# Optimization experiments

Measured on AMD Instinct MI355X. Metric: run time of the kernel, lower is better.

## Reference

```python
import jax, jax.numpy as jnp
import numpy as np

D_MODEL = 1024
N_HEADS = 16
HEAD_DIM = D_MODEL // N_HEADS


def setup_inputs() -> dict:
    key = jax.random.key(0)
    ks = jax.random.split(key, 5)
    T, B = 2048, 2
    scale = 1.0 / np.sqrt(D_MODEL)
    x = jax.random.normal(ks[0], (T, B, D_MODEL), dtype=jnp.float32)
    W_qkv = jax.random.normal(ks[1], (D_MODEL, 3 * D_MODEL), dtype=jnp.float32) * scale
    b_qkv = jnp.zeros((3 * D_MODEL,), dtype=jnp.float32)
    W_out = jax.random.normal(ks[2], (D_MODEL, D_MODEL), dtype=jnp.float32) * scale
    b_out = jnp.zeros((D_MODEL,), dtype=jnp.float32)
    return {"x": x, "W_qkv": W_qkv, "b_qkv": b_qkv, "W_out": W_out, "b_out": b_out}


def reference(x, W_qkv, b_qkv, W_out, b_out):
    T, B, D = x.shape
    H, Dh = N_HEADS, HEAD_DIM
    qkv = x @ W_qkv + b_qkv  # [T, B, 3D]
    q, k, v = jnp.split(qkv, 3, axis=-1)
    # [T, B, D] -> [B, H, T, Dh]
    def to_heads(t):
        return t.reshape(T, B, H, Dh).transpose(1, 2, 0, 3)
    q, k, v = to_heads(q), to_heads(k), to_heads(v)
    scores = jnp.einsum("bhqd,bhkd->bhqk", q, k) / jnp.sqrt(jnp.float32(Dh))
    causal = jnp.tril(jnp.ones((T, T), dtype=bool))  # True where attention allowed
    scores = jnp.where(causal, scores, -jnp.inf)
    attn = jax.nn.softmax(scores, axis=-1)
    context = jnp.einsum("bhqk,bhkd->bhqd", attn, v)  # [B, H, T, Dh]
    context = context.transpose(2, 0, 1, 3).reshape(T, B, D)  # [T, B, D]
    return context @ W_out + b_out
```

## Files before the change

kernel.cpp:

```cpp
#include <hip/hip_runtime.h>
#include <stdint.h>

#define T_SEQ 2048
#define BATCH 2
#define DMODEL 1024
#define NH 16
#define DH 64
#define M_ROWS (T_SEQ * BATCH)
#define N_QKV (3 * DMODEL)
#define BHQ (32 * T_SEQ)

typedef unsigned short u16;
using bf16x8 = __attribute__((ext_vector_type(8))) __bf16;
using f32x4  = __attribute__((ext_vector_type(4))) float;

__device__ __forceinline__ u16 f2bf(float f) {
    union { float f; uint32_t u; } v; v.f = f;
    uint32_t r = v.u + 0x7fffu + ((v.u >> 16) & 1u);
    return (u16)(r >> 16);
}

__device__ __forceinline__ uint32_t pack2(float a, float b) {
    union { float f; uint32_t u; } x, y; x.f = a; y.f = b;
    return (x.u >> 16) | (y.u & 0xffff0000u);
}

__device__ __forceinline__ float bf2f(u16 u) {
    union { uint32_t u; float f; } v; v.u = (uint32_t)u << 16;
    return v.f;
}

__device__ __forceinline__ void lds_load16(void* lds, const void* g) {
    auto lp = (__attribute__((address_space(3))) uint32_t*)(uint32_t)(uintptr_t)lds;
    auto gp = (const __attribute__((address_space(1))) uint32_t*)(uintptr_t)g;
    __builtin_amdgcn_global_load_lds(gp, lp, 16, 0, 0);
}

#define SCQ 0.18033688011112f


__global__ void cvt4_kernel(const float* __restrict__ in, u16* __restrict__ out, int n4) {
    int i = blockIdx.x * 256 + threadIdx.x;
    if (i < n4) {
        float4 v = ((const float4*)in)[i];
        union { u16 u[4]; uint2 d; } o;
        o.u[0] = f2bf(v.x); o.u[1] = f2bf(v.y); o.u[2] = f2bf(v.z); o.u[3] = f2bf(v.w);
        ((uint2*)out)[i] = o.d;
    }
}

__global__ void cvt_t2_kernel(const float* __restrict__ A, u16* __restrict__ oA,
                              const float* __restrict__ B, u16* __restrict__ oB) {
    __shared__ float t[32][33];
    const int R = 1024;
    const float* in; u16* out; int C, bx;
    if (blockIdx.x < 96) { in = A; out = oA; C = 3072; bx = blockIdx.x * 32; }
    else                 { in = B; out = oB; C = 1024; bx = (blockIdx.x - 96) * 32; }
    int by = blockIdx.y * 32;
    int tx = threadIdx.x & 31, ty = threadIdx.x >> 5;
#pragma unroll
    for (int rr = 0; rr < 32; rr += 8)
        t[ty + rr][tx] = in[(size_t)(by + ty + rr) * C + bx + tx];
    __syncthreads();
#pragma unroll
    for (int rr = 0; rr < 32; rr += 8)
        out[(size_t)(bx + ty + rr) * R + by + tx] = f2bf(t[tx][ty + rr]);
}


template<int EPI, int NF>
__global__ __launch_bounds__(256) void gemm_kernel(
    const u16* __restrict__ A, const u16* __restrict__ Bt,
    const float* __restrict__ bias,
    u16* __restrict__ outQ, u16* __restrict__ outK, u16* __restrict__ outV,
    float* __restrict__ outF,
    int M, int N, int K)
{
    __shared__ __align__(16) u16 lA[2][128 * 32];
    __shared__ __align__(16) u16 lB[2][NF * 32 * 32];

    const int tid  = threadIdx.x;
    const int bm   = blockIdx.y * 128;
    const int bn   = blockIdx.x * (NF * 32);
    const int lane = tid & 63;
    const int wid  = tid >> 6;
    const int wm   = (wid >> 1) * 64;
    const int wn   = (wid & 1) * (NF * 16);
    const int qr   = lane & 15;
    const int quad = lane >> 4;
    const int r4   = lane >> 2;
    const int c4   = (((lane & 3) ^ ((r4 >> 1) & 3))) * 8;
    const int sw   = (qr >> 1) & 3;

    f32x4 acc[4][NF];
#pragma unroll
    for (int i = 0; i < 4; i++)
#pragma unroll
        for (int j = 0; j < NF; j++) acc[i][j] = f32x4{0.f, 0.f, 0.f, 0.f};

#pragma unroll
    for (int cc = 0; cc < 2; cc++) {
        int c = wid + cc * 4;
        lds_load16(&lA[0][c * 512], &A[(size_t)(bm + 16 * c + r4) * K + c4]);
    }
#pragma unroll
    for (int c = wid; c < 2 * NF; c += 4)
        lds_load16(&lB[0][c * 512], &Bt[(size_t)(bn + 16 * c + r4) * K + c4]);

    int p = 0;
    for (int k0 = 0; k0 < K; k0 += 32, p ^= 1) {
        __syncthreads();
        if (k0 + 32 < K) {
            int nb = p ^ 1;
#pragma unroll
            for (int cc = 0; cc < 2; cc++) {
                int c = wid + cc * 4;
                lds_load16(&lA[nb][c * 512], &A[(size_t)(bm + 16 * c + r4) * K + k0 + 32 + c4]);
            }
#pragma unroll
            for (int c = wid; c < 2 * NF; c += 4)
                lds_load16(&lB[nb][c * 512], &Bt[(size_t)(bn + 16 * c + r4) * K + k0 + 32 + c4]);
        }

        bf16x8 af[4], bfr[NF];
#pragma unroll
        for (int i = 0; i < 4; i++)
            af[i] = *(const bf16x8*)&lA[p][(wm + i * 16 + qr) * 32 + ((quad ^ sw) * 8)];
#pragma unroll
        for (int j = 0; j < NF; j++)
            bfr[j] = *(const bf16x8*)&lB[p][(wn + j * 16 + qr) * 32 + ((quad ^ sw) * 8)];
#pragma unroll
        for (int i = 0; i < 4; i++)
#pragma unroll
            for (int j = 0; j < NF; j++)
                acc[i][j] = __builtin_amdgcn_mfma_f32_16x16x32_bf16(af[i], bfr[j], acc[i][j], 0, 0, 0);
    }

#pragma unroll
    for (int i = 0; i < 4; i++) {
#pragma unroll
        for (int j = 0; j < NF; j++) {
            int col = bn + wn + j * 16 + qr;
            float bv = bias[col];
#pragma unroll
            for (int r = 0; r < 4; r++) {
                int row = bm + wm + i * 16 + quad * 4 + r;
                float val = acc[i][j][r] + bv;
                if (EPI == 0) {
                    int t = row >> 1, b = row & 1;
                    int which = col >> 10;
                    int dm = col & 1023;
                    int h = dm >> 6, dh = dm & 63;
                    int bh = b * NH + h;
                    if (which == 0) {
                        outQ[((size_t)bh * T_SEQ + t) * DH + dh] = f2bf(val * SCQ);
                    } else if (which == 1) {
                        outK[((size_t)bh * T_SEQ + t) * DH + dh] = f2bf(val);
                    } else {
                        outV[((size_t)bh * DH + dh) * T_SEQ + t] = f2bf(val);
                    }
                } else {
                    outF[(size_t)row * N + col] = val;
                }
            }
        }
    }
}


__global__ __launch_bounds__(256) void attn_kernel(
    const u16* __restrict__ Qb, const u16* __restrict__ Kb,
    const u16* __restrict__ Vt,
    u16* __restrict__ Op, float* __restrict__ Lp)
{
    __shared__ __align__(16) u16 lK[2][64 * 64];
    __shared__ __align__(16) u16 lV[2][64 * 64];
    __shared__ __align__(16) u16 lP[4][16 * 64];

    const int bh   = blockIdx.x;
    const int y    = blockIdx.y;
    const int qt   = (y < 8) ? 15 - y : y - 8;
    const int seg  = blockIdx.z;
    const int tid  = threadIdx.x;
    const int lane = tid & 63;
    const int wid  = tid >> 6;
    const int qr   = lane & 15;
    const int quad = lane >> 4;
    const int sw   = qr & 7;

    const int srow = wid * 8 + (lane >> 3);
    const int scol = (((lane & 7) ^ ((lane >> 3) & 7))) * 8;

    const u16* Q  = Qb + (size_t)bh * T_SEQ * DH;
    const u16* Kp = Kb + (size_t)bh * T_SEQ * DH;
    const u16* Vp = Vt + (size_t)bh * DH * T_SEQ;

    const int q0 = qt * 128 + wid * 32;

    bf16x8 qf[2][2];
#pragma unroll
    for (int g = 0; g < 2; g++)
#pragma unroll
        for (int ks = 0; ks < 2; ks++)
            qf[g][ks] = *(const bf16x8*)&Q[(size_t)(q0 + g * 16 + qr) * DH + ks * 32 + quad * 8];

    bf16x8 onesf;
#pragma unroll
    for (int j = 0; j < 8; j++) onesf[j] = (__bf16)1.0f;

    f32x4 o[2][5];
#pragma unroll
    for (int g = 0; g < 2; g++)
#pragma unroll
        for (int f = 0; f < 5; f++) o[g][f] = f32x4{0.f, 0.f, 0.f, 0.f};

    const int kt0 = seg * (qt + 1);
    const int kt1 = kt0 + (qt + 1);

#pragma unroll
    for (int half = 0; half < 2; half++) {
        lds_load16(&lK[0][half * 2048 + wid * 512],
                   &Kp[(size_t)(kt0 * 64 + half * 32 + srow) * DH + scol]);
        lds_load16(&lV[0][half * 2048 + wid * 512],
                   &Vp[(size_t)(half * 32 + srow) * T_SEQ + kt0 * 64 + scol]);
    }

    int p = 0;
    for (int kt = kt0; kt < kt1; kt++, p ^= 1) {
        __syncthreads();
        if (kt + 1 < kt1) {
            int nb = p ^ 1;
#pragma unroll
            for (int half = 0; half < 2; half++) {
                lds_load16(&lK[nb][half * 2048 + wid * 512],
                           &Kp[(size_t)((kt + 1) * 64 + half * 32 + srow) * DH + scol]);
                lds_load16(&lV[nb][half * 2048 + wid * 512],
                           &Vp[(size_t)(half * 32 + srow) * T_SEQ + (kt + 1) * 64 + scol]);
            }
        }
        if (kt * 64 > q0 + 31) continue;

        f32x4 s[2][4];
#pragma unroll
        for (int g = 0; g < 2; g++)
#pragma unroll
            for (int fn = 0; fn < 4; fn++) s[g][fn] = f32x4{0.f, 0.f, 0.f, 0.f};
#pragma unroll
        for (int fn = 0; fn < 4; fn++)
#pragma unroll
            for (int ks = 0; ks < 2; ks++) {
                bf16x8 kf = *(const bf16x8*)&lK[p][(fn * 16 + qr) * 64 + (((ks * 4 + quad) ^ sw) * 8)];
#pragma unroll
                for (int g = 0; g < 2; g++)
                    s[g][fn] = __builtin_amdgcn_mfma_f32_16x16x32_bf16(kf, qf[g][ks], s[g][fn], 0, 0, 0);
            }

        if (kt * 64 + 63 > q0) {
#pragma unroll
            for (int g = 0; g < 2; g++) {
                int q = q0 + g * 16 + qr;
#pragma unroll
                for (int fn = 0; fn < 4; fn++) {
                    int key = kt * 64 + fn * 16 + quad * 4;
#pragma unroll
                    for (int r = 0; r < 4; r++)
                        if (key + r > q) s[g][fn][r] = -1e30f;
                }
            }
        }

        bf16x8 pf[2][2];
#pragma unroll
        for (int g = 0; g < 2; g++) {
#pragma unroll
            for (int fn = 0; fn < 4; fn++) {
                float p0 = exp2f(s[g][fn][0]);
                float p1 = exp2f(s[g][fn][1]);
                float p2 = exp2f(s[g][fn][2]);
                float p3 = exp2f(s[g][fn][3]);
                uint2 w; w.x = pack2(p0, p1); w.y = pack2(p2, p3);
                int phys = ((fn * 2 + (quad >> 1)) ^ sw);
                *(uint2*)&lP[wid][qr * 64 + phys * 8 + (quad & 1) * 4] = w;
            }
#pragma unroll
            for (int ks = 0; ks < 2; ks++)
                pf[g][ks] = *(const bf16x8*)&lP[wid][qr * 64 + (((ks * 4 + quad) ^ sw) * 8)];
        }

#pragma unroll
        for (int f = 0; f < 5; f++)
#pragma unroll
            for (int ks = 0; ks < 2; ks++) {
                bf16x8 vf = (f == 4) ? onesf
                    : *(const bf16x8*)&lV[p][(f * 16 + qr) * 64 + (((ks * 4 + quad) ^ sw) * 8)];
#pragma unroll
                for (int g = 0; g < 2; g++)
                    o[g][f] = __builtin_amdgcn_mfma_f32_16x16x32_bf16(vf, pf[g][ks], o[g][f], 0, 0, 0);
            }
    }

#pragma unroll
    for (int g = 0; g < 2; g++) {
        int q = q0 + g * 16 + qr;
        size_t rbase = (size_t)seg * BHQ + (size_t)bh * T_SEQ + q;
        if (quad == 0) Lp[rbase] = o[g][4][0];
#pragma unroll
        for (int f = 0; f < 4; f++) {
            uint2 w;
            w.x = (uint32_t)f2bf(o[g][f][0]) | ((uint32_t)f2bf(o[g][f][1]) << 16);
            w.y = (uint32_t)f2bf(o[g][f][2]) | ((uint32_t)f2bf(o[g][f][3]) << 16);
            *(uint2*)&Op[rbase * 64 + f * 16 + quad * 4] = w;
        }
    }
}


__global__ void merge_kernel(const u16* __restrict__ Op, const float* __restrict__ Lp,
                             u16* __restrict__ ctx)
{
    int idx = blockIdx.x * 256 + threadIdx.x;
    int fq  = idx & 15;
    int q   = (idx >> 4) & (T_SEQ - 1);
    int bh  = idx >> 15;
    int b = bh >> 4, h = bh & 15;
    size_t rbase = (size_t)bh * T_SEQ + q;

    float invl = 1.0f / (Lp[rbase] + Lp[rbase + BHQ]);
    union { uint2 d; u16 u[4]; } a, c, r;
    a.d = *(const uint2*)&Op[rbase * 64 + fq * 4];
    c.d = *(const uint2*)&Op[(rbase + BHQ) * 64 + fq * 4];
#pragma unroll
    for (int i = 0; i < 4; i++)
        r.u[i] = f2bf((bf2f(a.u[i]) + bf2f(c.u[i])) * invl);
    *(uint2*)&ctx[((size_t)q * BATCH + b) * DMODEL + h * DH + fq * 4] = r.d;
}


extern "C" void kernel_launch(void* const* d_in, const int* in_sizes, int n_in,
                              void* d_out, int out_size, void* d_ws, size_t ws_size,
                              hipStream_t stream) {
    const float* x     = (const float*)d_in[0];
    const float* W_qkv = (const float*)d_in[1];
    const float* b_qkv = (const float*)d_in[2];
    const float* W_out = (const float*)d_in[3];
    const float* b_out = (const float*)d_in[4];
    float* out = (float*)d_out;

    char* ws = (char*)d_ws;
    u16* xb     = (u16*)(ws + 0);
    u16* wqkv_t = (u16*)(ws + (8u  << 20));
    u16* wout_t = (u16*)(ws + (14u << 20));
    u16* Qb     = (u16*)(ws + (16u << 20));
    u16* Kb     = (u16*)(ws + (24u << 20));
    u16* Vt     = (u16*)(ws + (32u << 20));
    float* Lp   = (float*)(ws + (40u << 20));
    u16* ctx    = xb;
    u16* Op     = (u16*)d_out;

    cvt4_kernel  <<<(M_ROWS * DMODEL / 4) / 256, 256, 0, stream>>>(x, xb, M_ROWS * DMODEL / 4);
    cvt_t2_kernel<<<dim3(128, 32), 256, 0, stream>>>(W_qkv, wqkv_t, W_out, wout_t);

    gemm_kernel<0, 4><<<dim3(N_QKV / 128, M_ROWS / 128), 256, 0, stream>>>(
        xb, wqkv_t, b_qkv, Qb, Kb, Vt, nullptr, M_ROWS, N_QKV, DMODEL);

    attn_kernel<<<dim3(BATCH * NH, T_SEQ / 128, 2), 256, 0, stream>>>(
        Qb, Kb, Vt, Op, Lp);

    merge_kernel<<<(BHQ * 16) / 256, 256, 0, stream>>>(Op, Lp, ctx);

    gemm_kernel<1, 4><<<dim3(DMODEL / 128, M_ROWS / 128), 256, 0, stream>>>(
        ctx, wout_t, b_out, nullptr, nullptr, nullptr, out, M_ROWS, DMODEL, DMODEL);
}
```

Measured before the change: 190.7 us.

## Drop split-K attention and merge kernel; use 512-thread blocks writing context directly

```diff
diff --git a/kernel.cpp b/kernel.cpp
--- a/kernel.cpp
+++ b/kernel.cpp
@@ -8,7 +8,6 @@
 #define DH 64
 #define M_ROWS (T_SEQ * BATCH)
 #define N_QKV (3 * DMODEL)
-#define BHQ (32 * T_SEQ)
 
 typedef unsigned short u16;
 using bf16x8 = __attribute__((ext_vector_type(8))) __bf16;
@@ -39,32 +38,33 @@
 #define SCQ 0.18033688011112f
 
 
-__global__ void cvt4_kernel(const float* __restrict__ in, u16* __restrict__ out, int n4) {
-    int i = blockIdx.x * 256 + threadIdx.x;
-    if (i < n4) {
-        float4 v = ((const float4*)in)[i];
+__global__ void prep_kernel(const float* __restrict__ x, u16* __restrict__ xb,
+                            const float* __restrict__ Wq, u16* __restrict__ oq,
+                            const float* __restrict__ Wo, u16* __restrict__ oo) {
+    __shared__ float t[32][33];
+    if (blockIdx.x < 4096) {
+        int i = blockIdx.x * 256 + threadIdx.x;
+        float4 v = ((const float4*)x)[i];
         union { u16 u[4]; uint2 d; } o;
         o.u[0] = f2bf(v.x); o.u[1] = f2bf(v.y); o.u[2] = f2bf(v.z); o.u[3] = f2bf(v.w);
-        ((uint2*)out)[i] = o.d;
-    }
-}
-
-__global__ void cvt_t2_kernel(const float* __restrict__ A, u16* __restrict__ oA,
-                              const float* __restrict__ B, u16* __restrict__ oB) {
-    __shared__ float t[32][33];
-    const int R = 1024;
-    const float* in; u16* out; int C, bx;
-    if (blockIdx.x < 96) { in = A; out = oA; C = 3072; bx = blockIdx.x * 32; }
-    else                 { in = B; out = oB; C = 1024; bx = (blockIdx.x - 96) * 32; }
-    int by = blockIdx.y * 32;
-    int tx = threadIdx.x & 31, ty = threadIdx.x >> 5;
-#pragma unroll
-    for (int rr = 0; rr < 32; rr += 8)
-        t[ty + rr][tx] = in[(size_t)(by + ty + rr) * C + bx + tx];
-    __syncthreads();
-#pragma unroll
-    for (int rr = 0; rr < 32; rr += 8)
-        out[(size_t)(bx + ty + rr) * R + by + tx] = f2bf(t[tx][ty + rr]);
+        ((uint2*)xb)[i] = o.d;
+    } else {
+        const int R = 1024;
+        int bxx = blockIdx.x - 4096;
+        int gx = bxx & 127, gy = bxx >> 7;
+        const float* in; u16* out; int C, bx;
+        if (gx < 96) { in = Wq; out = oq; C = 3072; bx = gx * 32; }
+        else         { in = Wo; out = oo; C = 1024; bx = (gx - 96) * 32; }
+        int by = gy * 32;
+        int tx = threadIdx.x & 31, ty = threadIdx.x >> 5;
+#pragma unroll
+        for (int rr = 0; rr < 32; rr += 8)
+            t[ty + rr][tx] = in[(size_t)(by + ty + rr) * C + bx + tx];
+        __syncthreads();
+#pragma unroll
+        for (int rr = 0; rr < 32; rr += 8)
+            out[(size_t)(bx + ty + rr) * R + by + tx] = f2bf(t[tx][ty + rr]);
+    }
 }
 
 
@@ -168,19 +168,17 @@
 }
 
 
-__global__ __launch_bounds__(256) void attn_kernel(
+__global__ __launch_bounds__(512) void attn_kernel(
     const u16* __restrict__ Qb, const u16* __restrict__ Kb,
-    const u16* __restrict__ Vt,
-    u16* __restrict__ Op, float* __restrict__ Lp)
+    const u16* __restrict__ Vt, u16* __restrict__ ctx)
 {
     __shared__ __align__(16) u16 lK[2][64 * 64];
     __shared__ __align__(16) u16 lV[2][64 * 64];
-    __shared__ __align__(16) u16 lP[4][16 * 64];
+    __shared__ __align__(16) u16 lP[8][16 * 64];
 
     const int bh   = blockIdx.x;
     const int y    = blockIdx.y;
     const int qt   = (y < 8) ? 15 - y : y - 8;
-    const int seg  = blockIdx.z;
     const int tid  = threadIdx.x;
     const int lane = tid & 63;
     const int wid  = tid >> 6;
@@ -194,98 +192,74 @@
     const u16* Q  = Qb + (size_t)bh * T_SEQ * DH;
     const u16* Kp = Kb + (size_t)bh * T_SEQ * DH;
     const u16* Vp = Vt + (size_t)bh * DH * T_SEQ;
-
-    const int q0 = qt * 128 + wid * 32;
-
-    bf16x8 qf[2][2];
-#pragma unroll
-    for (int g = 0; g < 2; g++)
-#pragma unroll
-        for (int ks = 0; ks < 2; ks++)
-            qf[g][ks] = *(const bf16x8*)&Q[(size_t)(q0 + g * 16 + qr) * DH + ks * 32 + quad * 8];
+    const int b = bh >> 4, h = bh & 15;
+
+    const int q0 = qt * 128 + wid * 16;
+
+    bf16x8 qf[2];
+#pragma unroll
+    for (int ks = 0; ks < 2; ks++)
+        qf[ks] = *(const bf16x8*)&Q[(size_t)(q0 + qr) * DH + ks * 32 + quad * 8];
 
     bf16x8 onesf;
 #pragma unroll
     for (int j = 0; j < 8; j++) onesf[j] = (__bf16)1.0f;
 
-    f32x4 o[2][5];
-#pragma unroll
-    for (int g = 0; g < 2; g++)
-#pragma unroll
-        for (int f = 0; f < 5; f++) o[g][f] = f32x4{0.f, 0.f, 0.f, 0.f};
-
-    const int kt0 = seg * (qt + 1);
-    const int kt1 = kt0 + (qt + 1);
-
-#pragma unroll
-    for (int half = 0; half < 2; half++) {
-        lds_load16(&lK[0][half * 2048 + wid * 512],
-                   &Kp[(size_t)(kt0 * 64 + half * 32 + srow) * DH + scol]);
-        lds_load16(&lV[0][half * 2048 + wid * 512],
-                   &Vp[(size_t)(half * 32 + srow) * T_SEQ + kt0 * 64 + scol]);
-    }
+    f32x4 o[5];
+#pragma unroll
+    for (int f = 0; f < 5; f++) o[f] = f32x4{0.f, 0.f, 0.f, 0.f};
+
+    const int NT = 2 * (qt + 1);
+
+    lds_load16(&lK[0][wid * 512], &Kp[(size_t)srow * DH + scol]);
+    lds_load16(&lV[0][wid * 512], &Vp[(size_t)srow * T_SEQ + scol]);
 
     int p = 0;
-    for (int kt = kt0; kt < kt1; kt++, p ^= 1) {
+    for (int kt = 0; kt < NT; kt++, p ^= 1) {
         __syncthreads();
-        if (kt + 1 < kt1) {
+        if (kt + 1 < NT) {
             int nb = p ^ 1;
-#pragma unroll
-            for (int half = 0; half < 2; half++) {
-                lds_load16(&lK[nb][half * 2048 + wid * 512],
-                           &Kp[(size_t)((kt + 1) * 64 + half * 32 + srow) * DH + scol]);
-                lds_load16(&lV[nb][half * 2048 + wid * 512],
-                           &Vp[(size_t)(half * 32 + srow) * T_SEQ + (kt + 1) * 64 + scol]);
-            }
-        }
-        if (kt * 64 > q0 + 31) continue;
-
-        f32x4 s[2][4];
-#pragma unroll
-        for (int g = 0; g < 2; g++)
-#pragma unroll
-            for (int fn = 0; fn < 4; fn++) s[g][fn] = f32x4{0.f, 0.f, 0.f, 0.f};
+            lds_load16(&lK[nb][wid * 512], &Kp[(size_t)((kt + 1) * 64 + srow) * DH + scol]);
+            lds_load16(&lV[nb][wid * 512], &Vp[(size_t)srow * T_SEQ + (kt + 1) * 64 + scol]);
+        }
+        if (kt * 64 > q0 + 15) continue;
+
+        f32x4 s[4];
+#pragma unroll
+        for (int fn = 0; fn < 4; fn++) s[fn] = f32x4{0.f, 0.f, 0.f, 0.f};
 #pragma unroll
         for (int fn = 0; fn < 4; fn++)
 #pragma unroll
             for (int ks = 0; ks < 2; ks++) {
                 bf16x8 kf = *(const bf16x8*)&lK[p][(fn * 16 + qr) * 64 + (((ks * 4 + quad) ^ sw) * 8)];
-#pragma unroll
-                for (int g = 0; g < 2; g++)
-                    s[g][fn] = __builtin_amdgcn_mfma_f32_16x16x32_bf16(kf, qf[g][ks], s[g][fn], 0, 0, 0);
+                s[fn] = __builtin_amdgcn_mfma_f32_16x16x32_bf16(kf, qf[ks], s[fn], 0, 0, 0);
             }
 
         if (kt * 64 + 63 > q0) {
-#pragma unroll
-            for (int g = 0; g < 2; g++) {
-                int q = q0 + g * 16 + qr;
-#pragma unroll
-                for (int fn = 0; fn < 4; fn++) {
-                    int key = kt * 64 + fn * 16 + quad * 4;
-#pragma unroll
-                    for (int r = 0; r < 4; r++)
-                        if (key + r > q) s[g][fn][r] = -1e30f;
-                }
-            }
-        }
-
-        bf16x8 pf[2][2];
-#pragma unroll
-        for (int g = 0; g < 2; g++) {
+            int q = q0 + qr;
 #pragma unroll
             for (int fn = 0; fn < 4; fn++) {
-                float p0 = exp2f(s[g][fn][0]);
-                float p1 = exp2f(s[g][fn][1]);
-                float p2 = exp2f(s[g][fn][2]);
-                float p3 = exp2f(s[g][fn][3]);
-                uint2 w; w.x = pack2(p0, p1); w.y = pack2(p2, p3);
-                int phys = ((fn * 2 + (quad >> 1)) ^ sw);
-                *(uint2*)&lP[wid][qr * 64 + phys * 8 + (quad & 1) * 4] = w;
-            }
-#pragma unroll
-            for (int ks = 0; ks < 2; ks++)
-                pf[g][ks] = *(const bf16x8*)&lP[wid][qr * 64 + (((ks * 4 + quad) ^ sw) * 8)];
-        }
+                int key = kt * 64 + fn * 16 + quad * 4;
+#pragma unroll
+                for (int r = 0; r < 4; r++)
+                    if (key + r > q) s[fn][r] = -1e30f;
+            }
+        }
+
+        bf16x8 pf[2];
+#pragma unroll
+        for (int fn = 0; fn < 4; fn++) {
+            float p0 = exp2f(s[fn][0]);
+            float p1 = exp2f(s[fn][1]);
+            float p2 = exp2f(s[fn][2]);
+            float p3 = exp2f(s[fn][3]);
+            uint2 w; w.x = pack2(p0, p1); w.y = pack2(p2, p3);
+            int phys = ((fn * 2 + (quad >> 1)) ^ sw);
+            *(uint2*)&lP[wid][qr * 64 + phys * 8 + (quad & 1) * 4] = w;
+        }
+#pragma unroll
+        for (int ks = 0; ks < 2; ks++)
+            pf[ks] = *(const bf16x8*)&lP[wid][qr * 64 + (((ks * 4 + quad) ^ sw) * 8)];
 
 #pragma unroll
         for (int f = 0; f < 5; f++)
@@ -293,46 +267,21 @@
             for (int ks = 0; ks < 2; ks++) {
                 bf16x8 vf = (f == 4) ? onesf
                     : *(const bf16x8*)&lV[p][(f * 16 + qr) * 64 + (((ks * 4 + quad) ^ sw) * 8)];
-#pragma unroll
-                for (int g = 0; g < 2; g++)
-                    o[g][f] = __builtin_amdgcn_mfma_f32_16x16x32_bf16(vf, pf[g][ks], o[g][f], 0, 0, 0);
-            }
-    }
-
-#pragma unroll
-    for (int g = 0; g < 2; g++) {
-        int q = q0 + g * 16 + qr;
-        size_t rbase = (size_t)seg * BHQ + (size_t)bh * T_SEQ + q;
-        if (quad == 0) Lp[rbase] = o[g][4][0];
+                o[f] = __builtin_amdgcn_mfma_f32_16x16x32_bf16(vf, pf[ks], o[f], 0, 0, 0);
+            }
+    }
+
+    {
+        int q = q0 + qr;
+        float invl = 1.0f / o[4][0];
 #pragma unroll
         for (int f = 0; f < 4; f++) {
             uint2 w;
-            w.x = (uint32_t)f2bf(o[g][f][0]) | ((uint32_t)f2bf(o[g][f][1]) << 16);
-            w.y = (uint32_t)f2bf(o[g][f][2]) | ((uint32_t)f2bf(o[g][f][3]) << 16);
-            *(uint2*)&Op[rbase * 64 + f * 16 + quad * 4] = w;
-        }
-    }
-}
-
-
-__global__ void merge_kernel(const u16* __restrict__ Op, const float* __restrict__ Lp,
-                             u16* __restrict__ ctx)
-{
-    int idx = blockIdx.x * 256 + threadIdx.x;
-    int fq  = idx & 15;
-    int q   = (idx >> 4) & (T_SEQ - 1);
-    int bh  = idx >> 15;
-    int b = bh >> 4, h = bh & 15;
-    size_t rbase = (size_t)bh * T_SEQ + q;
-
-    float invl = 1.0f / (Lp[rbase] + Lp[rbase + BHQ]);
-    union { uint2 d; u16 u[4]; } a, c, r;
-    a.d = *(const uint2*)&Op[rbase * 64 + fq * 4];
-    c.d = *(const uint2*)&Op[(rbase + BHQ) * 64 + fq * 4];
-#pragma unroll
-    for (int i = 0; i < 4; i++)
-        r.u[i] = f2bf((bf2f(a.u[i]) + bf2f(c.u[i])) * invl);
-    *(uint2*)&ctx[((size_t)q * BATCH + b) * DMODEL + h * DH + fq * 4] = r.d;
+            w.x = (uint32_t)f2bf(o[f][0] * invl) | ((uint32_t)f2bf(o[f][1] * invl) << 16);
+            w.y = (uint32_t)f2bf(o[f][2] * invl) | ((uint32_t)f2bf(o[f][3] * invl) << 16);
+            *(uint2*)&ctx[((size_t)q * BATCH + b) * DMODEL + h * DH + f * 16 + quad * 4] = w;
+        }
+    }
 }
 
 
@@ -353,20 +302,15 @@
     u16* Qb     = (u16*)(ws + (16u << 20));
     u16* Kb     = (u16*)(ws + (24u << 20));
     u16* Vt     = (u16*)(ws + (32u << 20));
-    float* Lp   = (float*)(ws + (40u << 20));
     u16* ctx    = xb;
-    u16* Op     = (u16*)d_out;
-
-    cvt4_kernel  <<<(M_ROWS * DMODEL / 4) / 256, 256, 0, stream>>>(x, xb, M_ROWS * DMODEL / 4);
-    cvt_t2_kernel<<<dim3(128, 32), 256, 0, stream>>>(W_qkv, wqkv_t, W_out, wout_t);
+
+    prep_kernel<<<8192, 256, 0, stream>>>(x, xb, W_qkv, wqkv_t, W_out, wout_t);
 
     gemm_kernel<0, 4><<<dim3(N_QKV / 128, M_ROWS / 128), 256, 0, stream>>>(
         xb, wqkv_t, b_qkv, Qb, Kb, Vt, nullptr, M_ROWS, N_QKV, DMODEL);
 
-    attn_kernel<<<dim3(BATCH * NH, T_SEQ / 128, 2), 256, 0, stream>>>(
-        Qb, Kb, Vt, Op, Lp);
-
-    merge_kernel<<<(BHQ * 16) / 256, 256, 0, stream>>>(Op, Lp, ctx);
+    attn_kernel<<<dim3(BATCH * NH, T_SEQ / 128), 512, 0, stream>>>(
+        Qb, Kb, Vt, ctx);
 
     gemm_kernel<1, 4><<<dim3(DMODEL / 128, M_ROWS / 128), 256, 0, stream>>>(
         ctx, wout_t, b_out, nullptr, nullptr, nullptr, out, M_ROWS, DMODEL, DMODEL);
```

Measured after the change: 184.2 us. 3.4% less time.
